# Kernel optimization log

Hardware: AMD Instinct MI355X
Metric: run time of the kernel (lower is better)

## Reference

```python
import jax, jax.numpy as jnp
import numpy as np

BETA = 0.9
TH = 1.0
SLOPE = 25.0  # fast-sigmoid surrogate slope (spike_grad_slope)

@jax.custom_vjp
def spike_fn(m):
    # Heaviside on (mem - threshold)
    return (m > 0).astype(m.dtype)

def _spike_fwd(m):
    return spike_fn(m), m

def _spike_bwd(m, g):
    # fast-sigmoid surrogate gradient: 1 / (slope*|m| + 1)^2
    return (g / (SLOPE * jnp.abs(m) + 1.0) ** 2,)

spike_fn.defvjp(_spike_fwd, _spike_bwd)


def setup_inputs() -> dict:
    key = jax.random.key(0)
    k1, k2, k3 = jax.random.split(key, 3)
    T, B, I, H, O = 128, 8192, 2, 256, 2
    x = jax.random.normal(k1, (T, B, I), dtype=jnp.float32)
    # xavier_uniform with gain=1: limit = sqrt(6/(fan_in+fan_out))
    lim1 = float(np.sqrt(6.0 / (I + H)))
    lim2 = float(np.sqrt(6.0 / (H + O)))
    W1 = jax.random.uniform(k2, (H, I), jnp.float32, -lim1, lim1)
    W2 = jax.random.uniform(k3, (O, H), jnp.float32, -lim2, lim2)
    return {"x": x, "W1": W1, "W2": W2}


def reference(x, W1, W2):
    # Precompute all per-step input currents in one GEMM: [T,B,H]
    cur = jnp.einsum('tbi,hi->tbh', x, W1)
    B, H = cur.shape[1], cur.shape[2]
    mem0 = jnp.zeros((B, H), cur.dtype)

    def step(mem, c):
        # snntorch Leaky (reset_mechanism='subtract'):
        # reset based on PREVIOUS mem's spike, then leaky integrate, then fire
        reset = spike_fn(mem - TH)
        mem_new = BETA * mem + c - reset * TH
        spk = spike_fn(mem_new - TH)
        # original code detaches mem between steps (1-step truncated BPTT)
        return jax.lax.stop_gradient(mem_new), spk

    _, spk_rec = jax.lax.scan(step, mem0, cur)  # spk_rec: [T,B,H]
    spk_avg = spk_rec[-10:].mean(0)             # [B,H]
    out = jnp.einsum('bh,oh->bo', spk_avg, W2)  # [B,O]
    return out
```

## Files before the change

kernel.cpp:

```cpp
#include <hip/hip_runtime.h>


#define T_STEPS 128
#define BATCH   8192
#define HID     256
#define TAIL    10
#define RH      8
#define LB      64
#define NWAVE   4
#define HG      8

__global__ __launch_bounds__(256) void snn_scan(const float* __restrict__ x,
                                                const float* __restrict__ W1,
                                                const float* __restrict__ W2,
                                                float2* __restrict__ partial) {
    const int tid   = threadIdx.x;
    const int lane  = tid & 63;
    const int wave  = tid >> 6;
    const int hg    = blockIdx.x & (HG - 1);
    const int bg    = blockIdx.x >> 3;
    const int b     = bg * LB + lane;
    const int hbase = hg * (NWAVE * RH) + wave * RH;

    float w0[RH], w1[RH];
#pragma unroll
    for (int r = 0; r < RH; ++r) {
        w0[r] = W1[2 * (hbase + r)];
        w1[r] = W1[2 * (hbase + r) + 1];
    }

    const float2* xb = (const float2*)x + b;

    float mem[RH], spk[RH], cnt[RH];
#pragma unroll
    for (int r = 0; r < RH; ++r) { mem[r] = 0.0f; spk[r] = 0.0f; cnt[r] = 0.0f; }

#define STEP(r, xa, xc)                                                          \
    {                                                                            \
        const float c = __fadd_rn(__fmul_rn((xa), w0[r]), __fmul_rn((xc), w1[r]));\
        mem[r] = __fsub_rn(__fadd_rn(__fmul_rn(0.9f, mem[r]), c), spk[r]);       \
        spk[r] = (mem[r] > 1.0f) ? 1.0f : 0.0f;                                  \
    }

#pragma unroll 4
    for (int t = 0; t < T_STEPS - TAIL; ++t) {
        const float2 xv = xb[(size_t)t * BATCH];
#pragma unroll
        for (int r = 0; r < RH; ++r) STEP(r, xv.x, xv.y)
    }
#pragma unroll
    for (int t = T_STEPS - TAIL; t < T_STEPS; ++t) {
        const float2 xv = xb[(size_t)t * BATCH];
#pragma unroll
        for (int r = 0; r < RH; ++r) {
            STEP(r, xv.x, xv.y)
            cnt[r] += spk[r];
        }
    }
#undef STEP

    float p0 = 0.0f, p1 = 0.0f;
#pragma unroll
    for (int r = 0; r < RH; ++r) {
        const float avg = cnt[r] / 10.0f;
        p0 = __fadd_rn(p0, __fmul_rn(avg, W2[hbase + r]));
        p1 = __fadd_rn(p1, __fmul_rn(avg, W2[HID + hbase + r]));
    }

    __shared__ float2 red[NWAVE][LB];
    red[wave][lane] = make_float2(p0, p1);
    __syncthreads();
    if (wave == 0) {
        const float2 a0 = red[0][lane], a1 = red[1][lane];
        const float2 a2 = red[2][lane], a3 = red[3][lane];
        float2 s;
        s.x = __fadd_rn(__fadd_rn(a0.x, a1.x), __fadd_rn(a2.x, a3.x));
        s.y = __fadd_rn(__fadd_rn(a0.y, a1.y), __fadd_rn(a2.y, a3.y));
        partial[(size_t)hg * BATCH + b] = s;
    }
}

__global__ __launch_bounds__(256) void snn_reduce(const float2* __restrict__ partial,
                                                  float2* __restrict__ out) {
    const int b = blockIdx.x * 256 + threadIdx.x;
    float sx = 0.0f, sy = 0.0f;
#pragma unroll
    for (int hg = 0; hg < HG; ++hg) {
        const float2 p = partial[(size_t)hg * BATCH + b];
        sx = __fadd_rn(sx, p.x);
        sy = __fadd_rn(sy, p.y);
    }
    out[b] = make_float2(sx, sy);
}

extern "C" void kernel_launch(void* const* d_in, const int* in_sizes, int n_in,
                              void* d_out, int out_size, void* d_ws, size_t ws_size,
                              hipStream_t stream) {
    const float* x  = (const float*)d_in[0];
    const float* W1 = (const float*)d_in[1];
    const float* W2 = (const float*)d_in[2];
    float2* out     = (float2*)d_out;
    float2* partial = (float2*)d_ws;

    snn_scan<<<(BATCH / LB) * HG, 256, 0, stream>>>(x, W1, W2, partial);
    snn_reduce<<<BATCH / 256, 256, 0, stream>>>(partial, out);
}
```

Baseline: 105.1 us.

## Software-prefetch x with rolling register buffer and remap block indices

```diff
diff --git a/kernel.cpp b/kernel.cpp
--- a/kernel.cpp
+++ b/kernel.cpp
@@ -9,6 +9,8 @@
 #define LB      64
 #define NWAVE   4
 #define HG      8
+#define NBG     (BATCH / LB)
+#define PF      8
 
 __global__ __launch_bounds__(256) void snn_scan(const float* __restrict__ x,
                                                 const float* __restrict__ W1,
@@ -17,8 +19,8 @@
     const int tid   = threadIdx.x;
     const int lane  = tid & 63;
     const int wave  = tid >> 6;
-    const int hg    = blockIdx.x & (HG - 1);
-    const int bg    = blockIdx.x >> 3;
+    const int bg    = blockIdx.x & (NBG - 1);
+    const int hg    = blockIdx.x >> 7;
     const int b     = bg * LB + lane;
     const int hbase = hg * (NWAVE * RH) + wave * RH;
 
@@ -35,22 +37,43 @@
 #pragma unroll
     for (int r = 0; r < RH; ++r) { mem[r] = 0.0f; spk[r] = 0.0f; cnt[r] = 0.0f; }
 
-#define STEP(r, xa, xc)                                                          \
-    {                                                                            \
+#define STEP(r, xa, xc)                                                           \
+    {                                                                             \
         const float c = __fadd_rn(__fmul_rn((xa), w0[r]), __fmul_rn((xc), w1[r]));\
-        mem[r] = __fsub_rn(__fadd_rn(__fmul_rn(0.9f, mem[r]), c), spk[r]);       \
-        spk[r] = (mem[r] > 1.0f) ? 1.0f : 0.0f;                                  \
+        mem[r] = __fsub_rn(__fadd_rn(__fmul_rn(0.9f, mem[r]), c), spk[r]);        \
+        spk[r] = (mem[r] > 1.0f) ? 1.0f : 0.0f;                                   \
     }
 
-#pragma unroll 4
-    for (int t = 0; t < T_STEPS - TAIL; ++t) {
-        const float2 xv = xb[(size_t)t * BATCH];
+    float2 buf[PF];
 #pragma unroll
-        for (int r = 0; r < RH; ++r) STEP(r, xv.x, xv.y)
+    for (int j = 0; j < PF; ++j) buf[j] = xb[(size_t)j * BATCH];
+
+    for (int tb = 0; tb < T_STEPS - 2 * PF; tb += PF) {
+#pragma unroll
+        for (int j = 0; j < PF; ++j) {
+            const float2 xv = buf[j];
+            buf[j] = xb[(size_t)(tb + PF + j) * BATCH];
+#pragma unroll
+            for (int r = 0; r < RH; ++r) STEP(r, xv.x, xv.y)
+        }
+    }
+
+    float2 buf2[PF];
+#pragma unroll
+    for (int j = 0; j < PF; ++j) buf2[j] = xb[(size_t)(T_STEPS - PF + j) * BATCH];
+
+#pragma unroll
+    for (int j = 0; j < PF; ++j) {
+        const float2 xv = buf[j];
+#pragma unroll
+        for (int r = 0; r < RH; ++r) {
+            STEP(r, xv.x, xv.y)
+            if (j >= PF - 2) cnt[r] += spk[r];
+        }
     }
 #pragma unroll
-    for (int t = T_STEPS - TAIL; t < T_STEPS; ++t) {
-        const float2 xv = xb[(size_t)t * BATCH];
+    for (int j = 0; j < PF; ++j) {
+        const float2 xv = buf2[j];
 #pragma unroll
         for (int r = 0; r < RH; ++r) {
             STEP(r, xv.x, xv.y)
@@ -102,6 +125,6 @@
     float2* out     = (float2*)d_out;
     float2* partial = (float2*)d_ws;
 
-    snn_scan<<<(BATCH / LB) * HG, 256, 0, stream>>>(x, W1, W2, partial);
+    snn_scan<<<NBG * HG, 256, 0, stream>>>(x, W1, W2, partial);
     snn_reduce<<<BATCH / 256, 256, 0, stream>>>(partial, out);
 }
```

New measurement: 103.1 us. Within noise of the previous version (-1.9%).
